# Kernel optimization log

Measured on AMD Instinct MI355X. Metric: run time of the kernel, lower is better.

Reference implementation:

```python
import jax, jax.numpy as jnp
import numpy as np

EPS = 1e-8
CLAMP = 1.0 - 1e-5
C = 1.0  # curvature


def _norm(x):
    return jnp.sqrt(jnp.sum(x * x, axis=-1, keepdims=True))


def clamp_to_ball(x, c=C):
    max_norm = CLAMP / c ** 0.5
    n = jnp.maximum(_norm(x), EPS)
    scale = jnp.where(n > max_norm, max_norm / n, 1.0)
    return x * scale


def logmap0(x, c=C):
    n = jnp.maximum(_norm(x), EPS)
    sc = c ** 0.5
    a = jnp.minimum(sc * n, 1.0 - EPS)
    return jnp.arctanh(a) / (sc * n) * x


def expmap0(v, c=C):
    n = jnp.maximum(_norm(v), EPS)
    sc = c ** 0.5
    t = jnp.minimum(sc * n, 15.0)
    return clamp_to_ball(jnp.tanh(t) * v / (sc * n), c)


def mobius_add(x, y, c=C):
    x2 = jnp.sum(x * x, -1, keepdims=True)
    y2 = jnp.sum(y * y, -1, keepdims=True)
    xy = jnp.sum(x * y, -1, keepdims=True)
    num = (1 + 2 * c * xy + c * y2) * x + (1 - c * x2) * y
    den = 1 + 2 * c * xy + c * c * x2 * y2
    return clamp_to_ball(num / jnp.maximum(den, EPS), c)


def hyp_linear(x, W, b, c=C):
    out = expmap0(logmap0(x, c) @ W.T, c)
    bias_ball = expmap0(b[None, :], c)
    return mobius_add(out, jnp.broadcast_to(bias_ball, out.shape), c)


def pairwise_poincare_dist(Q, K, c=C):
    # Q, K: [B, h, T, dk]. Distance d(q,k) = 2/sqrt(c) * atanh(sqrt(c)*||(-q) (+) k||).
    # ||num||^2 of mobius_add(-q, k) depends only on scalars |q|^2, |k|^2, q.k,
    # so we avoid the (B,h,T,T,dk) expansion while computing identical math.
    q2 = jnp.sum(Q * Q, -1)[..., :, None]          # [B,h,T,1]
    k2 = jnp.sum(K * K, -1)[..., None, :]          # [B,h,1,T]
    xy = -jnp.einsum('bhtd,bhsd->bhts', Q, K)      # (-q).k
    A = 1 + 2 * c * xy + c * k2
    Bc = 1 - c * q2
    num2 = A * A * q2 + Bc * Bc * k2 + 2 * A * Bc * xy
    den = jnp.maximum(1 + 2 * c * xy + c * c * q2 * k2, EPS)
    n = jnp.sqrt(jnp.maximum(num2, 0.0)) / den
    n = jnp.minimum(n, CLAMP / c ** 0.5)           # clamp_to_ball on the diff vector
    n = jnp.minimum(n, 1.0 - EPS)                  # .clamp(max=1-EPS)
    sc = c ** 0.5
    return 2.0 / sc * jnp.arctanh(sc * n)


def setup_inputs() -> dict:
    key = jax.random.key(0)
    ks = jax.random.split(key, 10)
    B, T, d = 4, 1024, 512
    x = expmap0(0.05 * jax.random.normal(ks[0], (B, T, d), jnp.float32))
    a = (6.0 / (d + d)) ** 0.5  # xavier uniform bound
    def w(k):
        return jax.random.uniform(k, (d, d), jnp.float32, -a, a)
    return {
        'x': x,
        'Wq': w(ks[1]), 'bq': 0.01 * jax.random.normal(ks[2], (d,), jnp.float32),
        'Wk': w(ks[3]), 'bk': 0.01 * jax.random.normal(ks[4], (d,), jnp.float32),
        'Wv': w(ks[5]), 'bv': 0.01 * jax.random.normal(ks[6], (d,), jnp.float32),
        'Wo': w(ks[7]), 'bo': 0.01 * jax.random.normal(ks[8], (d,), jnp.float32),
    }


def reference(x, Wq, bq, Wk, bk, Wv, bv, Wo, bo):
    B, T, d = x.shape
    h = 8
    dk = d // h
    x_eucl = logmap0(x, C)
    Q = hyp_linear(x, Wq, bq, C)
    K = hyp_linear(x, Wk, bk, C)
    V = x_eucl @ Wv.T + bv
    Q = Q.reshape(B, T, h, dk).transpose(0, 2, 1, 3)
    K = K.reshape(B, T, h, dk).transpose(0, 2, 1, 3)
    V = V.reshape(B, T, h, dk).transpose(0, 2, 1, 3)
    dists = pairwise_poincare_dist(Q, K, C)        # [B,h,T,T]
    scores = -dists / (dk ** 0.5)
    attn = jax.nn.softmax(scores, axis=-1)
    out = jnp.einsum('bhts,bhsd->bhtd', attn, V)
    out = out.transpose(0, 2, 1, 3).reshape(B, T, d)
    return out @ Wo.T + bo
```

## Files before the change

kernel.cpp:

```cpp
#include <hip/hip_runtime.h>
#include <math.h>

#define EPSF   1e-8f
#define CLAMPF 0.99999f

typedef __attribute__((ext_vector_type(8))) short bf16x8;
typedef __attribute__((ext_vector_type(4))) float f32x4;
#define MFMA16(a,b,c) __builtin_amdgcn_mfma_f32_16x16x32_bf16(a,b,c,0,0,0)

__device__ __forceinline__ unsigned cvt_pk_bf16(float lo, float hi) {
  unsigned r;
  asm("v_cvt_pk_bf16_f32 %0, %1, %2" : "=v"(r) : "v"(lo), "v"(hi));
  return r;
}

typedef __attribute__((address_space(1))) const void GV;
typedef __attribute__((address_space(3))) void LV;
__device__ __forceinline__ void gload_lds16(const void* g, void* l) {
  __builtin_amdgcn_global_load_lds((GV*)g, (LV*)l, 16, 0, 0);
}

__device__ __forceinline__ float wave_sum64(float v) {
  v += __shfl_xor(v, 1, 64);
  v += __shfl_xor(v, 2, 64);
  v += __shfl_xor(v, 4, 64);
  v += __shfl_xor(v, 8, 64);
  v += __shfl_xor(v, 16, 64);
  v += __shfl_xor(v, 32, 64);
  return v;
}

__global__ __launch_bounds__(256) void prep_logmap(const float* __restrict__ x,
                                                   const float* __restrict__ Wq,
                                                   const float* __restrict__ Wk,
                                                   const float* __restrict__ Wv,
                                                   const float* __restrict__ Wo,
                                                   const float* __restrict__ bq,
                                                   const float* __restrict__ bk,
                                                   short* __restrict__ xe,
                                                   short* __restrict__ Wqbf,
                                                   short* __restrict__ Wkbf,
                                                   short* __restrict__ Wvbf,
                                                   short* __restrict__ Wobf,
                                                   float* __restrict__ bb) {
  const int id = blockIdx.x;
  const int t = threadIdx.x;
  __shared__ float red[4];
  if (id < 2048) {
    const int half = t >> 7, tc = t & 127;
    const int row = id * 2 + half;
    float4 v = ((const float4*)(x + (size_t)row * 512))[tc];
    float s = wave_sum64(v.x * v.x + v.y * v.y + v.z * v.z + v.w * v.w);
    if ((t & 63) == 0) red[t >> 6] = s;
    __syncthreads();
    float n2 = red[half * 2] + red[half * 2 + 1];
    float n = sqrtf(n2);
    float nm = fmaxf(n, EPSF);
    float a = fminf(nm, 1.0f);
    float at = 0.5f * logf((1.f + a) / (1.f - a));
    float sc = at / nm;
    uint2 o;
    o.x = cvt_pk_bf16(v.x * sc, v.y * sc);
    o.y = cvt_pk_bf16(v.z * sc, v.w * sc);
    ((uint2*)(xe + (size_t)row * 512))[tc] = o;
    return;
  }
  const int wid = id - 2048;
  if (wid < 512) {
    const int which = wid >> 7, chunk = wid & 127;
    const float* src; short* dst;
    switch (which) {
      case 0: src = Wq; dst = Wqbf; break;
      case 1: src = Wk; dst = Wkbf; break;
      case 2: src = Wv; dst = Wvbf; break;
      default: src = Wo; dst = Wobf; break;
    }
    const int idx = chunk * 2048 + t * 8;
    float4 a = *(const float4*)(src + idx);
    float4 b2 = *(const float4*)(src + idx + 4);
    union { int4 v; unsigned u[4]; } o;
    o.u[0] = cvt_pk_bf16(a.x, a.y);
    o.u[1] = cvt_pk_bf16(a.z, a.w);
    o.u[2] = cvt_pk_bf16(b2.x, b2.y);
    o.u[3] = cvt_pk_bf16(b2.z, b2.w);
    *(int4*)(dst + idx) = o.v;
    return;
  }
  const int which = wid - 512;
  const float* b = which ? bk : bq;
  float* o = bb + (size_t)which * 520;
  float2 v = ((const float2*)b)[t];
  float s = wave_sum64(v.x * v.x + v.y * v.y);
  if ((t & 63) == 0) red[t >> 6] = s;
  __syncthreads();
  float n2 = red[0] + red[1] + red[2] + red[3];
  float n = sqrtf(n2);
  float nm = fmaxf(n, EPSF);
  float tt = fminf(nm, 15.f);
  float f = tanhf(tt) / nm;
  float on = f * nm;
  if (on > CLAMPF) f *= CLAMPF / on;
  ((float2*)o)[t] = make_float2(f * v.x, f * v.y);
  if (t == 0) o[512] = f * f * n2;
}

template <int VT>
__device__ __forceinline__ void gemm_core128(const short* __restrict__ A,
                                             const short* __restrict__ W,
                                             const float* __restrict__ bias,
                                             void* __restrict__ outp,
                                             int bx, int by) {
  __shared__ __align__(16) short As[128][64];
  __shared__ __align__(16) short Ws[64][64];
  const int t = threadIdx.x;
  const int wave = t >> 6, lane = t & 63, lg = lane >> 4, lr = lane & 15;
  const int mh = wave & 1, nh = wave >> 1;
  f32x4 z = {0.f, 0.f, 0.f, 0.f};
  f32x4 acc[4][2];
#pragma unroll
  for (int i = 0; i < 4; ++i) { acc[i][0] = z; acc[i][1] = z; }

  const int rsub = lane >> 3;
  const int swz = ((lane & 7) ^ rsub) * 8;
  const short* Ag0 = A + (size_t)(by * 128 + wave * 32 + rsub) * 512 + swz;
  const short* Wg0 = W + (size_t)(bx * 64 + wave * 16 + rsub) * 512 + swz;
  short* Al0 = &As[wave * 32][0];
  short* Al1 = &As[wave * 32 + 8][0];
  short* Al2 = &As[wave * 32 + 16][0];
  short* Al3 = &As[wave * 32 + 24][0];
  short* Wl0 = &Ws[wave * 16][0];
  short* Wl1 = &Ws[wave * 16 + 8][0];

  const int rb = nh * 32 + lr;
  const int cx = (lr & 7) * 8;

  for (int kt = 0; kt < 512; kt += 64) {
    __syncthreads();
    gload_lds16(Ag0 + kt, Al0);
    gload_lds16(Ag0 + kt + 8 * 512, Al1);
    gload_lds16(Ag0 + kt + 16 * 512, Al2);
    gload_lds16(Ag0 + kt + 24 * 512, Al3);
    gload_lds16(Wg0 + kt, Wl0);
    gload_lds16(Wg0 + kt + 8 * 512, Wl1);
    __syncthreads();
#pragma unroll
    for (int kk = 0; kk < 2; ++kk) {
      const int c = (kk * 32 + lg * 8) ^ cx;
      bf16x8 bf0 = *(const bf16x8*)&Ws[rb][c];
      bf16x8 bf1 = *(const bf16x8*)&Ws[rb + 16][c];
#pragma unroll
      for (int i = 0; i < 4; ++i) {
        bf16x8 af = *(const bf16x8*)&As[mh * 64 + i * 16 + lr][c];
        acc[i][0] = MFMA16(af, bf0, acc[i][0]);
        acc[i][1] = MFMA16(af, bf1, acc[i][1]);
      }
    }
  }

  if (VT == 0) {
    float* out = (float*)outp;
    float b0 = 0.f, b1 = 0.f;
    if (bias) { b0 = bias[bx * 64 + nh * 32 + lr]; b1 = bias[bx * 64 + nh * 32 + 16 + lr]; }
#pragma unroll
    for (int i = 0; i < 4; ++i) {
#pragma unroll
      for (int r = 0; r < 4; ++r) {
        size_t row = (size_t)(by * 128 + mh * 64 + i * 16 + lg * 4 + r);
        out[row * 512 + bx * 64 + nh * 32 + lr]      = acc[i][0][r] + b0;
        out[row * 512 + bx * 64 + nh * 32 + 16 + lr] = acc[i][1][r] + b1;
      }
    }
  } else {
    short* vt = (short*)outp;
    const int bidx = by >> 3;
    const int tokb = (by & 7) * 128 + mh * 64;
    const int c0 = bx * 64 + nh * 32 + lr;
    const int c1 = c0 + 16;
    const float b0 = bias[c0], b1 = bias[c1];
    size_t base0 = ((size_t)(bidx * 8 + (c0 >> 6)) * 64 + (c0 & 63)) * 1024;
    size_t base1 = ((size_t)(bidx * 8 + (c1 >> 6)) * 64 + (c1 & 63)) * 1024;
#pragma unroll
    for (int i = 0; i < 4; ++i) {
      const int tok0 = tokb + i * 16 + lg * 4;
      uint2 pk;
      pk.x = cvt_pk_bf16(acc[i][0][0] + b0, acc[i][0][1] + b0);
      pk.y = cvt_pk_bf16(acc[i][0][2] + b0, acc[i][0][3] + b0);
      *(uint2*)(vt + base0 + tok0) = pk;
      pk.x = cvt_pk_bf16(acc[i][1][0] + b1, acc[i][1][1] + b1);
      pk.y = cvt_pk_bf16(acc[i][1][2] + b1, acc[i][1][3] + b1);
      *(uint2*)(vt + base1 + tok0) = pk;
    }
  }
}

__device__ __forceinline__ void gemm_core64(const short* __restrict__ A,
                                            const short* __restrict__ W,
                                            const float* __restrict__ bias,
                                            float* __restrict__ out,
                                            int bx, int by) {
  __shared__ __align__(16) short As[64][64];
  __shared__ __align__(16) short Ws[64][64];
  const int t = threadIdx.x;
  const int wave = t >> 6, lane = t & 63, lg = lane >> 4, lr = lane & 15;
  const int mh = wave & 1, nh = wave >> 1;
  f32x4 z = {0.f, 0.f, 0.f, 0.f};
  f32x4 acc00 = z, acc01 = z, acc10 = z, acc11 = z;

  const int rsub = lane >> 3;
  const int swz = ((lane & 7) ^ rsub) * 8;
  const short* Ag0 = A + (size_t)(by * 64 + wave * 16 + rsub) * 512 + swz;
  const short* Ag1 = Ag0 + 8 * 512;
  const short* Wg0 = W + (size_t)(bx * 64 + wave * 16 + rsub) * 512 + swz;
  const short* Wg1 = Wg0 + 8 * 512;
  short* Al0 = &As[wave * 16][0];
  short* Al1 = &As[wave * 16 + 8][0];
  short* Wl0 = &Ws[wave * 16][0];
  short* Wl1 = &Ws[wave * 16 + 8][0];

  const int ra = mh * 32 + lr;
  const int rb = nh * 32 + lr;
  const int cx = (lr & 7) * 8;

  for (int kt = 0; kt < 512; kt += 64) {
    __syncthreads();
    gload_lds16(Ag0 + kt, Al0);
    gload_lds16(Ag1 + kt, Al1);
    gload_lds16(Wg0 + kt, Wl0);
    gload_lds16(Wg1 + kt, Wl1);
    __syncthreads();
#pragma unroll
    for (int kk = 0; kk < 2; ++kk) {
      const int c = (kk * 32 + lg * 8) ^ cx;
      bf16x8 af0 = *(const bf16x8*)&As[ra][c];
      bf16x8 af1 = *(const bf16x8*)&As[ra + 16][c];
      bf16x8 bf0 = *(const bf16x8*)&Ws[rb][c];
      bf16x8 bf1 = *(const bf16x8*)&Ws[rb + 16][c];
      acc00 = MFMA16(af0, bf0, acc00);
      acc01 = MFMA16(af0, bf1, acc01);
      acc10 = MFMA16(af1, bf0, acc10);
      acc11 = MFMA16(af1, bf1, acc11);
    }
  }

  float b0 = 0.f, b1 = 0.f;
  if (bias) { b0 = bias[bx * 64 + nh * 32 + lr]; b1 = bias[bx * 64 + nh * 32 + 16 + lr]; }
#pragma unroll
  for (int r = 0; r < 4; ++r) {
    size_t row0 = (size_t)(by * 64 + mh * 32 + lg * 4 + r);
    size_t row1 = row0 + 16;
    out[row0 * 512 + bx * 64 + nh * 32 + lr] = acc00[r] + b0;
    out[row0 * 512 + bx * 64 + nh * 32 + 16 + lr] = acc01[r] + b1;
    out[row1 * 512 + bx * 64 + nh * 32 + lr] = acc10[r] + b0;
    out[row1 * 512 + bx * 64 + nh * 32 + 16 + lr] = acc11[r] + b1;
  }
}

__global__ __launch_bounds__(256) void gemm_qkv(const short* __restrict__ A,
                                                const short* __restrict__ Wq,
                                                const short* __restrict__ Wk,
                                                const short* __restrict__ Wv,
                                                const float* __restrict__ bv,
                                                float* __restrict__ Qo,
                                                float* __restrict__ Ko,
                                                short* __restrict__ Vt) {
  switch (blockIdx.z) {
    case 0: gemm_core128<0>(A, Wq, nullptr, Qo, blockIdx.x, blockIdx.y); break;
    case 1: gemm_core128<0>(A, Wk, nullptr, Ko, blockIdx.x, blockIdx.y); break;
    default: gemm_core128<1>(A, Wv, bv, Vt, blockIdx.x, blockIdx.y); break;
  }
}

__global__ __launch_bounds__(256) void gemm_bf(const short* __restrict__ A,
                                               const short* __restrict__ W,
                                               const float* __restrict__ bias,
                                               float* __restrict__ out) {
  gemm_core64(A, W, bias, out, blockIdx.x, blockIdx.y);
}

__global__ __launch_bounds__(256) void hyp_epilogue_v4(const float* __restrict__ Qb,
                                                       const float* __restrict__ Kb,
                                                       const float* __restrict__ bbase,
                                                       short* __restrict__ Qbf,
                                                       short* __restrict__ Kbf,
                                                       float* __restrict__ q2h,
                                                       float* __restrict__ k2h) {
  const int which = blockIdx.y;
  const float* Y = which ? Kb : Qb;
  const float* bb = bbase + (size_t)which * 520;
  short* Ybf = which ? Kbf : Qbf;
  float* y2h = which ? k2h : q2h;
  const int t = threadIdx.x;
  const int half = t >> 7, tc = t & 127;
  const int row = blockIdx.x * 2 + half;

  float4 y = ((const float4*)(Y + (size_t)row * 512))[tc];
  float4 w = ((const float4*)bb)[tc];
  __shared__ float red[8];
  float sn = wave_sum64(y.x * y.x + y.y * y.y + y.z * y.z + y.w * y.w);
  float sd = wave_sum64(y.x * w.x + y.y * w.y + y.z * w.z + y.w * w.w);
  if ((t & 63) == 0) { red[t >> 6] = sn; red[4 + (t >> 6)] = sd; }
  __syncthreads();
  float n2 = red[half * 2] + red[half * 2 + 1];
  float dt = red[4 + half * 2] + red[4 + half * 2 + 1];
  float y2 = bb[512];
  float n = sqrtf(n2);
  float nm = fmaxf(n, EPSF);
  float tt = fminf(nm, 15.f);
  float f = tanhf(tt) / nm;
  float on = f * nm;
  if (on > CLAMPF) f *= CLAMPF / on;
  float x2 = f * f * n2;
  float xy = f * dt;
  float A = 1.f + 2.f * xy + y2;
  float Bc = 1.f - x2;
  float den = fmaxf(1.f + 2.f * xy + x2 * y2, EPSF);
  float num2 = A * A * x2 + Bc * Bc * y2 + 2.f * A * Bc * xy;
  float nn = sqrtf(fmaxf(num2, 0.f)) / den;
  float nnm = fmaxf(nn, EPSF);
  float s2 = (nnm > CLAMPF) ? (CLAMPF / nnm) : 1.f;
  float g = s2 / den;
  float ox = g * (A * f * y.x + Bc * w.x);
  float oy = g * (A * f * y.y + Bc * w.y);
  float oz = g * (A * f * y.z + Bc * w.z);
  float ow = g * (A * f * y.w + Bc * w.w);
  uint2 o;
  o.x = cvt_pk_bf16(ox, oy);
  o.y = cvt_pk_bf16(oz, ow);
  ((uint2*)(Ybf + (size_t)row * 512))[tc] = o;
  float hs = ox * ox + oy * oy + oz * oz + ow * ow;
  hs += __shfl_xor(hs, 1, 64);
  hs += __shfl_xor(hs, 2, 64);
  hs += __shfl_xor(hs, 4, 64);
  hs += __shfl_xor(hs, 8, 64);
  if ((tc & 15) == 0) y2h[(size_t)(tc >> 4) * 4096 + row] = hs;
}

__global__ __launch_bounds__(512, 2) void attn_mfma_v8(const short* __restrict__ Qbf,
                                                       const short* __restrict__ Kbf,
                                                       const float* __restrict__ q2h,
                                                       const float* __restrict__ k2h,
                                                       const short* __restrict__ Vt,
                                                       short* __restrict__ Obf) {
  __shared__ __align__(16) short Ks[64][72];
  __shared__ __align__(16) short Vs[64][72];
  __shared__ __align__(16) float k2s[64];
  __shared__ __align__(16) float Ls[4][16][68];
  __shared__ float lsb[4][16];

  const int t = threadIdx.x;
  const int id = blockIdx.x;
  const int qt = id >> 5;
  const int pr = (((id >> 3) & 3) << 3) | (id & 7);
  const int hd = pr & 7, b = pr >> 3;
  const int wave = t >> 6, lane = t & 63, lg = lane >> 4, lr = lane & 15;
  const int qh = wave >> 1, kh = wave & 1;

  const size_t qrow = (size_t)(b * 1024 + qt * 64 + qh * 16 + lr);
  const bf16x8 qf0 = *(const bf16x8*)(Qbf + qrow * 512 + hd * 64 + lg * 8);
  const bf16x8 qf1 = *(const bf16x8*)(Qbf + qrow * 512 + hd * 64 + 32 + lg * 8);

  const float q2 = q2h[(size_t)hd * 4096 + b * 1024 + qt * 64 + qh * 16 + lr];
  const float bc = 1.f - q2;
  const float q2p1 = 1.f + q2;
  const float Xmin = 0.125f * (-17.6096137f - __builtin_amdgcn_logf(bc));

  const int sr = t >> 3, q8 = t & 7;
  const int p32 = sr & 31;
  const int kwr = (sr & 32) | (((p32 >> 2) & 1) << 4) | (((p32 >> 3) & 3) << 2) | (p32 & 3);
  const short* kgp = Kbf + (size_t)(b * 1024 + sr) * 512 + hd * 64 + q8 * 8;
  const short* vgp = Vt + ((size_t)(b * 8 + hd) * 64 + sr) * 1024 + q8 * 8;
  const float* k2gp = k2h + (size_t)hd * 4096 + b * 1024 + t;

  int4 rk0 = *(const int4*)kgp;
  int4 rv0 = *(const int4*)vgp;
  float rk2 = (t < 64) ? (1.f - *k2gp) : 0.f;

  f32x4 z = {0.f, 0.f, 0.f, 0.f};
  f32x4 acc0 = z, acc1 = z, acc2 = z, acc3 = z;
  float ls = 0.f;
  const int krow = kh * 32 + lr;
  const int kcol = kh * 32 + lg * 8;

  for (int kt = 0; kt < 16; ++kt) {
    __syncthreads();
    *(int4*)&Ks[kwr][q8 * 8] = rk0;
    *(int4*)&Vs[sr][q8 * 8] = rv0;
    if (t < 64) k2s[t] = rk2;
    __syncthreads();
    if (kt < 15) {
      kgp += 64 * 512; vgp += 64; k2gp += 64;
      rk0 = *(const int4*)kgp;
      rv0 = *(const int4*)vgp;
      if (t < 64) rk2 = 1.f - *k2gp;
    }

    bf16x8 kf0 = *(const bf16x8*)&Ks[krow][lg * 8];
    bf16x8 kf1 = *(const bf16x8*)&Ks[krow][32 + lg * 8];
    bf16x8 kg0 = *(const bf16x8*)&Ks[krow + 16][lg * 8];
    bf16x8 kg1 = *(const bf16x8*)&Ks[krow + 16][32 + lg * 8];
    __builtin_amdgcn_s_setprio(1);
    f32x4 sA = MFMA16(kf0, qf0, z);
    sA = MFMA16(kf1, qf1, sA);
    f32x4 sB = MFMA16(kg0, qf0, z);
    sB = MFMA16(kg1, qf1, sB);
    __builtin_amdgcn_s_setprio(0);

    float pA[4], pB[4];
#pragma unroll
    for (int r = 0; r < 4; ++r) {
      float d = sA[r];
      float mk = k2s[kh * 32 + lg * 8 + r];
      float den = fmaxf(fmaf(-2.f, d, fmaf(-q2, mk, q2p1)), EPSF);
      float t1 = fmaxf(fmaf(-bc, mk, den), 0.f);
      float sq = __builtin_amdgcn_sqrtf(den * t1);
      float vv = den + sq;
      float wv = mk * den;
      float X = fmaf(0.125f, __builtin_amdgcn_logf(wv),
                     -0.25f * __builtin_amdgcn_logf(vv));
      pA[r] = __builtin_amdgcn_exp2f(fmaxf(X, Xmin));
    }
#pragma unroll
    for (int r = 0; r < 4; ++r) {
      float d = sB[r];
      float mk = k2s[kh * 32 + lg * 8 + 4 + r];
      float den = fmaxf(fmaf(-2.f, d, fmaf(-q2, mk, q2p1)), EPSF);
      float t1 = fmaxf(fmaf(-bc, mk, den), 0.f);
      float sq = __builtin_amdgcn_sqrtf(den * t1);
      float vv = den + sq;
      float wv = mk * den;
      float X = fmaf(0.125f, __builtin_amdgcn_logf(wv),
                     -0.25f * __builtin_amdgcn_logf(vv));
      pB[r] = __builtin_amdgcn_exp2f(fmaxf(X, Xmin));
    }
    ls += (pA[0] + pA[1] + pA[2] + pA[3]) + (pB[0] + pB[1] + pB[2] + pB[3]);

    union { unsigned u[4]; bf16x8 v; } pf;
    pf.u[0] = cvt_pk_bf16(pA[0], pA[1]);
    pf.u[1] = cvt_pk_bf16(pA[2], pA[3]);
    pf.u[2] = cvt_pk_bf16(pB[0], pB[1]);
    pf.u[3] = cvt_pk_bf16(pB[2], pB[3]);

    bf16x8 v0 = *(const bf16x8*)&Vs[lr][kcol];
    bf16x8 v1 = *(const bf16x8*)&Vs[16 + lr][kcol];
    bf16x8 v2 = *(const bf16x8*)&Vs[32 + lr][kcol];
    bf16x8 v3 = *(const bf16x8*)&Vs[48 + lr][kcol];
    __builtin_amdgcn_s_setprio(1);
    acc0 = MFMA16(v0, pf.v, acc0);
    acc1 = MFMA16(v1, pf.v, acc1);
    acc2 = MFMA16(v2, pf.v, acc2);
    acc3 = MFMA16(v3, pf.v, acc3);
    __builtin_amdgcn_s_setprio(0);
  }

  ls += __shfl_xor(ls, 16, 64);
  ls += __shfl_xor(ls, 32, 64);

  if (kh == 1) {
    float* Lq = &Ls[qh][lr][0];
    *(f32x4*)(Lq + lg * 4) = acc0;
    *(f32x4*)(Lq + 16 + lg * 4) = acc1;
    *(f32x4*)(Lq + 32 + lg * 4) = acc2;
    *(f32x4*)(Lq + 48 + lg * 4) = acc3;
    if (lg == 0) lsb[qh][lr] = ls;
  }
  __syncthreads();
  if (kh == 0) {
    const float* Lq = &Ls[qh][lr][0];
    acc0 += *(const f32x4*)(Lq + lg * 4);
    acc1 += *(const f32x4*)(Lq + 16 + lg * 4);
    acc2 += *(const f32x4*)(Lq + 32 + lg * 4);
    acc3 += *(const f32x4*)(Lq + 48 + lg * 4);
    float inv = 1.f / (ls + lsb[qh][lr]);
    short* ob = Obf + qrow * 512 + hd * 64 + lg * 4;
    uint2 pk;
    pk.x = cvt_pk_bf16(acc0[0] * inv, acc0[1] * inv);
    pk.y = cvt_pk_bf16(acc0[2] * inv, acc0[3] * inv);
    *(uint2*)(ob) = pk;
    pk.x = cvt_pk_bf16(acc1[0] * inv, acc1[1] * inv);
    pk.y = cvt_pk_bf16(acc1[2] * inv, acc1[3] * inv);
    *(uint2*)(ob + 16) = pk;
    pk.x = cvt_pk_bf16(acc2[0] * inv, acc2[1] * inv);
    pk.y = cvt_pk_bf16(acc2[2] * inv, acc2[3] * inv);
    *(uint2*)(ob + 32) = pk;
    pk.x = cvt_pk_bf16(acc3[0] * inv, acc3[1] * inv);
    pk.y = cvt_pk_bf16(acc3[2] * inv, acc3[3] * inv);
    *(uint2*)(ob + 48) = pk;
  }
}

extern "C" void kernel_launch(void* const* d_in, const int* in_sizes, int n_in,
                              void* d_out, int out_size, void* d_ws, size_t ws_size,
                              hipStream_t stream) {
  const float* x  = (const float*)d_in[0];
  const float* Wq = (const float*)d_in[1];
  const float* bq = (const float*)d_in[2];
  const float* Wk = (const float*)d_in[3];
  const float* bk = (const float*)d_in[4];
  const float* Wv = (const float*)d_in[5];
  const float* bv = (const float*)d_in[6];
  const float* Wo = (const float*)d_in[7];
  const float* bo = (const float*)d_in[8];
  float* out = (float*)d_out;
  float* ws  = (float*)d_ws;

  const size_t M1 = 1048576ull;
  float* Qb    = ws;
  float* Kb    = ws + 2 * M1;
  short* Vt    = (short*)(ws + 4 * M1);
  short* xe_bf = (short*)(ws + 5 * M1);
  short* Qbf   = (short*)(ws + 5 * M1);
  short* Wqbf  = (short*)(ws + 6 * M1);
  short* Wkbf  = (short*)(ws + 6 * M1 + 131072);
  short* Wvbf  = (short*)(ws + 6 * M1 + 262144);
  short* Wobf  = (short*)(ws + 6 * M1 + 393216);
  short* attn_out = (short*)(ws + 6 * M1 + 524288);
  short* Kbf = (short*)out;
  float* bb  = out + M1;
  float* q2h = out + M1 + 2048;
  float* k2h = out + M1 + 2048 + 32768;

  hipLaunchKernelGGL(prep_logmap, dim3(2562), dim3(256), 0, stream,
                     x, Wq, Wk, Wv, Wo, bq, bk, xe_bf, Wqbf, Wkbf, Wvbf, Wobf, bb);

  hipLaunchKernelGGL(gemm_qkv, dim3(8, 32, 3), dim3(256), 0, stream,
                     xe_bf, Wqbf, Wkbf, Wvbf, bv, Qb, Kb, Vt);

  hipLaunchKernelGGL(hyp_epilogue_v4, dim3(2048, 2), dim3(256), 0, stream,
                     Qb, Kb, bb, Qbf, Kbf, q2h, k2h);

  hipLaunchKernelGGL(attn_mfma_v8, dim3(512), dim3(512), 0, stream,
                     Qbf, Kbf, q2h, k2h, Vt, attn_out);

  hipLaunchKernelGGL(gemm_bf, dim3(8, 64), dim3(256), 0, stream, attn_out, Wobf, bo, out);
}
```

Before: 67.83 us.

## Give each attention wave two query sub-tiles to reuse K/V fragments

The attention kernel drops from 512 to 256 threads per block, and each wave now handles two 16-row query sub-tiles instead of one. Each K and V fragment read from shared memory therefore feeds twice as many MFMAs, and per-thread global loads double to cover the same 64x64 tile. This cuts LDS reads and waves per query tile but raises register pressure (eight accumulators) and leaves fewer waves per block to hide latency.

```diff
diff --git a/kernel.cpp b/kernel.cpp
--- a/kernel.cpp
+++ b/kernel.cpp
@@ -335,7 +335,7 @@
   if ((tc & 15) == 0) y2h[(size_t)(tc >> 4) * 4096 + row] = hs;
 }
 
-__global__ __launch_bounds__(512, 2) void attn_mfma_v8(const short* __restrict__ Qbf,
+__global__ __launch_bounds__(256, 4) void attn_mfma_v9(const short* __restrict__ Qbf,
                                                        const short* __restrict__ Kbf,
                                                        const float* __restrict__ q2h,
                                                        const float* __restrict__ k2h,
@@ -353,44 +353,55 @@
   const int pr = (((id >> 3) & 3) << 3) | (id & 7);
   const int hd = pr & 7, b = pr >> 3;
   const int wave = t >> 6, lane = t & 63, lg = lane >> 4, lr = lane & 15;
-  const int qh = wave >> 1, kh = wave & 1;
-
-  const size_t qrow = (size_t)(b * 1024 + qt * 64 + qh * 16 + lr);
-  const bf16x8 qf0 = *(const bf16x8*)(Qbf + qrow * 512 + hd * 64 + lg * 8);
-  const bf16x8 qf1 = *(const bf16x8*)(Qbf + qrow * 512 + hd * 64 + 32 + lg * 8);
-
-  const float q2 = q2h[(size_t)hd * 4096 + b * 1024 + qt * 64 + qh * 16 + lr];
-  const float bc = 1.f - q2;
-  const float q2p1 = 1.f + q2;
-  const float Xmin = 0.125f * (-17.6096137f - __builtin_amdgcn_logf(bc));
-
-  const int sr = t >> 3, q8 = t & 7;
+  const int qp = wave >> 1, kh = wave & 1;
+
+  const size_t qrow0 = (size_t)(b * 1024 + qt * 64 + qp * 32 + lr);
+  const bf16x8 qf00 = *(const bf16x8*)(Qbf + qrow0 * 512 + hd * 64 + lg * 8);
+  const bf16x8 qf01 = *(const bf16x8*)(Qbf + qrow0 * 512 + hd * 64 + 32 + lg * 8);
+  const bf16x8 qf10 = *(const bf16x8*)(Qbf + (qrow0 + 16) * 512 + hd * 64 + lg * 8);
+  const bf16x8 qf11 = *(const bf16x8*)(Qbf + (qrow0 + 16) * 512 + hd * 64 + 32 + lg * 8);
+
+  const float q2a = q2h[(size_t)hd * 4096 + b * 1024 + qt * 64 + qp * 32 + lr];
+  const float q2b = q2h[(size_t)hd * 4096 + b * 1024 + qt * 64 + qp * 32 + 16 + lr];
+  const float bcA = 1.f - q2a, bcB = 1.f - q2b;
+  const float q2p1A = 1.f + q2a, q2p1B = 1.f + q2b;
+  const float XminA = 0.125f * (-17.6096137f - __builtin_amdgcn_logf(bcA));
+  const float XminB = 0.125f * (-17.6096137f - __builtin_amdgcn_logf(bcB));
+
+  const int sr = t >> 2, q4 = t & 3;
   const int p32 = sr & 31;
   const int kwr = (sr & 32) | (((p32 >> 2) & 1) << 4) | (((p32 >> 3) & 3) << 2) | (p32 & 3);
-  const short* kgp = Kbf + (size_t)(b * 1024 + sr) * 512 + hd * 64 + q8 * 8;
-  const short* vgp = Vt + ((size_t)(b * 8 + hd) * 64 + sr) * 1024 + q8 * 8;
+  const short* kgp = Kbf + (size_t)(b * 1024 + sr) * 512 + hd * 64 + q4 * 16;
+  const short* vgp = Vt + ((size_t)(b * 8 + hd) * 64 + sr) * 1024 + q4 * 16;
   const float* k2gp = k2h + (size_t)hd * 4096 + b * 1024 + t;
 
   int4 rk0 = *(const int4*)kgp;
+  int4 rk1 = *(const int4*)(kgp + 8);
   int4 rv0 = *(const int4*)vgp;
+  int4 rv1 = *(const int4*)(vgp + 8);
   float rk2 = (t < 64) ? (1.f - *k2gp) : 0.f;
 
   f32x4 z = {0.f, 0.f, 0.f, 0.f};
-  f32x4 acc0 = z, acc1 = z, acc2 = z, acc3 = z;
-  float ls = 0.f;
+  f32x4 aA0 = z, aA1 = z, aA2 = z, aA3 = z;
+  f32x4 aB0 = z, aB1 = z, aB2 = z, aB3 = z;
+  float lsA = 0.f, lsB = 0.f;
   const int krow = kh * 32 + lr;
   const int kcol = kh * 32 + lg * 8;
 
   for (int kt = 0; kt < 16; ++kt) {
     __syncthreads();
-    *(int4*)&Ks[kwr][q8 * 8] = rk0;
-    *(int4*)&Vs[sr][q8 * 8] = rv0;
+    *(int4*)&Ks[kwr][q4 * 16] = rk0;
+    *(int4*)&Ks[kwr][q4 * 16 + 8] = rk1;
+    *(int4*)&Vs[sr][q4 * 16] = rv0;
+    *(int4*)&Vs[sr][q4 * 16 + 8] = rv1;
     if (t < 64) k2s[t] = rk2;
     __syncthreads();
     if (kt < 15) {
       kgp += 64 * 512; vgp += 64; k2gp += 64;
       rk0 = *(const int4*)kgp;
+      rk1 = *(const int4*)(kgp + 8);
       rv0 = *(const int4*)vgp;
+      rv1 = *(const int4*)(vgp + 8);
       if (t < 64) rk2 = 1.f - *k2gp;
     }
 
@@ -399,92 +410,147 @@
     bf16x8 kg0 = *(const bf16x8*)&Ks[krow + 16][lg * 8];
     bf16x8 kg1 = *(const bf16x8*)&Ks[krow + 16][32 + lg * 8];
     __builtin_amdgcn_s_setprio(1);
-    f32x4 sA = MFMA16(kf0, qf0, z);
-    sA = MFMA16(kf1, qf1, sA);
-    f32x4 sB = MFMA16(kg0, qf0, z);
-    sB = MFMA16(kg1, qf1, sB);
+    f32x4 sA0 = MFMA16(kf0, qf00, z);
+    sA0 = MFMA16(kf1, qf01, sA0);
+    f32x4 sB0 = MFMA16(kg0, qf00, z);
+    sB0 = MFMA16(kg1, qf01, sB0);
+    f32x4 sA1 = MFMA16(kf0, qf10, z);
+    sA1 = MFMA16(kf1, qf11, sA1);
+    f32x4 sB1 = MFMA16(kg0, qf10, z);
+    sB1 = MFMA16(kg1, qf11, sB1);
     __builtin_amdgcn_s_setprio(0);
 
-    float pA[4], pB[4];
+    float mkA[4], mkB[4];
 #pragma unroll
     for (int r = 0; r < 4; ++r) {
-      float d = sA[r];
-      float mk = k2s[kh * 32 + lg * 8 + r];
-      float den = fmaxf(fmaf(-2.f, d, fmaf(-q2, mk, q2p1)), EPSF);
-      float t1 = fmaxf(fmaf(-bc, mk, den), 0.f);
-      float sq = __builtin_amdgcn_sqrtf(den * t1);
-      float vv = den + sq;
-      float wv = mk * den;
-      float X = fmaf(0.125f, __builtin_amdgcn_logf(wv),
-                     -0.25f * __builtin_amdgcn_logf(vv));
-      pA[r] = __builtin_amdgcn_exp2f(fmaxf(X, Xmin));
-    }
+      mkA[r] = k2s[kh * 32 + lg * 8 + r];
+      mkB[r] = k2s[kh * 32 + lg * 8 + 4 + r];
+    }
+
+    float pA0[4], pB0[4], pA1[4], pB1[4];
 #pragma unroll
     for (int r = 0; r < 4; ++r) {
-      float d = sB[r];
-      float mk = k2s[kh * 32 + lg * 8 + 4 + r];
-      float den = fmaxf(fmaf(-2.f, d, fmaf(-q2, mk, q2p1)), EPSF);
-      float t1 = fmaxf(fmaf(-bc, mk, den), 0.f);
-      float sq = __builtin_amdgcn_sqrtf(den * t1);
-      float vv = den + sq;
-      float wv = mk * den;
-      float X = fmaf(0.125f, __builtin_amdgcn_logf(wv),
-                     -0.25f * __builtin_amdgcn_logf(vv));
-      pB[r] = __builtin_amdgcn_exp2f(fmaxf(X, Xmin));
-    }
-    ls += (pA[0] + pA[1] + pA[2] + pA[3]) + (pB[0] + pB[1] + pB[2] + pB[3]);
-
-    union { unsigned u[4]; bf16x8 v; } pf;
-    pf.u[0] = cvt_pk_bf16(pA[0], pA[1]);
-    pf.u[1] = cvt_pk_bf16(pA[2], pA[3]);
-    pf.u[2] = cvt_pk_bf16(pB[0], pB[1]);
-    pf.u[3] = cvt_pk_bf16(pB[2], pB[3]);
+      {
+        float den = fmaxf(fmaf(-2.f, sA0[r], fmaf(-q2a, mkA[r], q2p1A)), EPSF);
+        float t1 = fmaxf(fmaf(-bcA, mkA[r], den), 0.f);
+        float sq = __builtin_amdgcn_sqrtf(den * t1);
+        float X = fmaf(0.125f, __builtin_amdgcn_logf(mkA[r] * den),
+                       -0.25f * __builtin_amdgcn_logf(den + sq));
+        pA0[r] = __builtin_amdgcn_exp2f(fmaxf(X, XminA));
+      }
+      {
+        float den = fmaxf(fmaf(-2.f, sB0[r], fmaf(-q2a, mkB[r], q2p1A)), EPSF);
+        float t1 = fmaxf(fmaf(-bcA, mkB[r], den), 0.f);
+        float sq = __builtin_amdgcn_sqrtf(den * t1);
+        float X = fmaf(0.125f, __builtin_amdgcn_logf(mkB[r] * den),
+                       -0.25f * __builtin_amdgcn_logf(den + sq));
+        pB0[r] = __builtin_amdgcn_exp2f(fmaxf(X, XminA));
+      }
+      {
+        float den = fmaxf(fmaf(-2.f, sA1[r], fmaf(-q2b, mkA[r], q2p1B)), EPSF);
+        float t1 = fmaxf(fmaf(-bcB, mkA[r], den), 0.f);
+        float sq = __builtin_amdgcn_sqrtf(den * t1);
+        float X = fmaf(0.125f, __builtin_amdgcn_logf(mkA[r] * den),
+                       -0.25f * __builtin_amdgcn_logf(den + sq));
+        pA1[r] = __builtin_amdgcn_exp2f(fmaxf(X, XminB));
+      }
+      {
+        float den = fmaxf(fmaf(-2.f, sB1[r], fmaf(-q2b, mkB[r], q2p1B)), EPSF);
+        float t1 = fmaxf(fmaf(-bcB, mkB[r], den), 0.f);
+        float sq = __builtin_amdgcn_sqrtf(den * t1);
+        float X = fmaf(0.125f, __builtin_amdgcn_logf(mkB[r] * den),
+                       -0.25f * __builtin_amdgcn_logf(den + sq));
+        pB1[r] = __builtin_amdgcn_exp2f(fmaxf(X, XminB));
+      }
+    }
+    lsA += (pA0[0] + pA0[1] + pA0[2] + pA0[3]) + (pB0[0] + pB0[1] + pB0[2] + pB0[3]);
+    lsB += (pA1[0] + pA1[1] + pA1[2] + pA1[3]) + (pB1[0] + pB1[1] + pB1[2] + pB1[3]);
+
+    union { unsigned u[4]; bf16x8 v; } pf0, pf1;
+    pf0.u[0] = cvt_pk_bf16(pA0[0], pA0[1]);
+    pf0.u[1] = cvt_pk_bf16(pA0[2], pA0[3]);
+    pf0.u[2] = cvt_pk_bf16(pB0[0], pB0[1]);
+    pf0.u[3] = cvt_pk_bf16(pB0[2], pB0[3]);
+    pf1.u[0] = cvt_pk_bf16(pA1[0], pA1[1]);
+    pf1.u[1] = cvt_pk_bf16(pA1[2], pA1[3]);
+    pf1.u[2] = cvt_pk_bf16(pB1[0], pB1[1]);
+    pf1.u[3] = cvt_pk_bf16(pB1[2], pB1[3]);
 
     bf16x8 v0 = *(const bf16x8*)&Vs[lr][kcol];
     bf16x8 v1 = *(const bf16x8*)&Vs[16 + lr][kcol];
     bf16x8 v2 = *(const bf16x8*)&Vs[32 + lr][kcol];
     bf16x8 v3 = *(const bf16x8*)&Vs[48 + lr][kcol];
     __builtin_amdgcn_s_setprio(1);
-    acc0 = MFMA16(v0, pf.v, acc0);
-    acc1 = MFMA16(v1, pf.v, acc1);
-    acc2 = MFMA16(v2, pf.v, acc2);
-    acc3 = MFMA16(v3, pf.v, acc3);
+    aA0 = MFMA16(v0, pf0.v, aA0);
+    aA1 = MFMA16(v1, pf0.v, aA1);
+    aA2 = MFMA16(v2, pf0.v, aA2);
+    aA3 = MFMA16(v3, pf0.v, aA3);
+    aB0 = MFMA16(v0, pf1.v, aB0);
+    aB1 = MFMA16(v1, pf1.v, aB1);
+    aB2 = MFMA16(v2, pf1.v, aB2);
+    aB3 = MFMA16(v3, pf1.v, aB3);
     __builtin_amdgcn_s_setprio(0);
   }
 
-  ls += __shfl_xor(ls, 16, 64);
-  ls += __shfl_xor(ls, 32, 64);
+  lsA += __shfl_xor(lsA, 16, 64);
+  lsA += __shfl_xor(lsA, 32, 64);
+  lsB += __shfl_xor(lsB, 16, 64);
+  lsB += __shfl_xor(lsB, 32, 64);
 
   if (kh == 1) {
-    float* Lq = &Ls[qh][lr][0];
-    *(f32x4*)(Lq + lg * 4) = acc0;
-    *(f32x4*)(Lq + 16 + lg * 4) = acc1;
-    *(f32x4*)(Lq + 32 + lg * 4) = acc2;
-    *(f32x4*)(Lq + 48 + lg * 4) = acc3;
-    if (lg == 0) lsb[qh][lr] = ls;
+    float* Lq0 = &Ls[qp * 2][lr][0];
+    *(f32x4*)(Lq0 + lg * 4) = aA0;
+    *(f32x4*)(Lq0 + 16 + lg * 4) = aA1;
+    *(f32x4*)(Lq0 + 32 + lg * 4) = aA2;
+    *(f32x4*)(Lq0 + 48 + lg * 4) = aA3;
+    float* Lq1 = &Ls[qp * 2 + 1][lr][0];
+    *(f32x4*)(Lq1 + lg * 4) = aB0;
+    *(f32x4*)(Lq1 + 16 + lg * 4) = aB1;
+    *(f32x4*)(Lq1 + 32 + lg * 4) = aB2;
+    *(f32x4*)(Lq1 + 48 + lg * 4) = aB3;
+    if (lg == 0) { lsb[qp * 2][lr] = lsA; lsb[qp * 2 + 1][lr] = lsB; }
   }
   __syncthreads();
   if (kh == 0) {
-    const float* Lq = &Ls[qh][lr][0];
-    acc0 += *(const f32x4*)(Lq + lg * 4);
-    acc1 += *(const f32x4*)(Lq + 16 + lg * 4);
-    acc2 += *(const f32x4*)(Lq + 32 + lg * 4);
-    acc3 += *(const f32x4*)(Lq + 48 + lg * 4);
-    float inv = 1.f / (ls + lsb[qh][lr]);
-    short* ob = Obf + qrow * 512 + hd * 64 + lg * 4;
+    const float* Lq0 = &Ls[qp * 2][lr][0];
+    aA0 += *(const f32x4*)(Lq0 + lg * 4);
+    aA1 += *(const f32x4*)(Lq0 + 16 + lg * 4);
+    aA2 += *(const f32x4*)(Lq0 + 32 + lg * 4);
+    aA3 += *(const f32x4*)(Lq0 + 48 + lg * 4);
+    const float* Lq1 = &Ls[qp * 2 + 1][lr][0];
+    aB0 += *(const f32x4*)(Lq1 + lg * 4);
+    aB1 += *(const f32x4*)(Lq1 + 16 + lg * 4);
+    aB2 += *(const f32x4*)(Lq1 + 32 + lg * 4);
+    aB3 += *(const f32x4*)(Lq1 + 48 + lg * 4);
+    float invA = 1.f / (lsA + lsb[qp * 2][lr]);
+    float invB = 1.f / (lsB + lsb[qp * 2 + 1][lr]);
+    short* ob0 = Obf + qrow0 * 512 + hd * 64 + lg * 4;
+    short* ob1 = Obf + (qrow0 + 16) * 512 + hd * 64 + lg * 4;
     uint2 pk;
-    pk.x = cvt_pk_bf16(acc0[0] * inv, acc0[1] * inv);
-    pk.y = cvt_pk_bf16(acc0[2] * inv, acc0[3] * inv);
-    *(uint2*)(ob) = pk;
-    pk.x = cvt_pk_bf16(acc1[0] * inv, acc1[1] * inv);
-    pk.y = cvt_pk_bf16(acc1[2] * inv, acc1[3] * inv);
-    *(uint2*)(ob + 16) = pk;
-    pk.x = cvt_pk_bf16(acc2[0] * inv, acc2[1] * inv);
-    pk.y = cvt_pk_bf16(acc2[2] * inv, acc2[3] * inv);
-    *(uint2*)(ob + 32) = pk;
-    pk.x = cvt_pk_bf16(acc3[0] * inv, acc3[1] * inv);
-    pk.y = cvt_pk_bf16(acc3[2] * inv, acc3[3] * inv);
-    *(uint2*)(ob + 48) = pk;
+    pk.x = cvt_pk_bf16(aA0[0] * invA, aA0[1] * invA);
+    pk.y = cvt_pk_bf16(aA0[2] * invA, aA0[3] * invA);
+    *(uint2*)(ob0) = pk;
+    pk.x = cvt_pk_bf16(aA1[0] * invA, aA1[1] * invA);
+    pk.y = cvt_pk_bf16(aA1[2] * invA, aA1[3] * invA);
+    *(uint2*)(ob0 + 16) = pk;
+    pk.x = cvt_pk_bf16(aA2[0] * invA, aA2[1] * invA);
+    pk.y = cvt_pk_bf16(aA2[2] * invA, aA2[3] * invA);
+    *(uint2*)(ob0 + 32) = pk;
+    pk.x = cvt_pk_bf16(aA3[0] * invA, aA3[1] * invA);
+    pk.y = cvt_pk_bf16(aA3[2] * invA, aA3[3] * invA);
+    *(uint2*)(ob0 + 48) = pk;
+    pk.x = cvt_pk_bf16(aB0[0] * invB, aB0[1] * invB);
+    pk.y = cvt_pk_bf16(aB0[2] * invB, aB0[3] * invB);
+    *(uint2*)(ob1) = pk;
+    pk.x = cvt_pk_bf16(aB1[0] * invB, aB1[1] * invB);
+    pk.y = cvt_pk_bf16(aB1[2] * invB, aB1[3] * invB);
+    *(uint2*)(ob1 + 16) = pk;
+    pk.x = cvt_pk_bf16(aB2[0] * invB, aB2[1] * invB);
+    pk.y = cvt_pk_bf16(aB2[2] * invB, aB2[3] * invB);
+    *(uint2*)(ob1 + 32) = pk;
+    pk.x = cvt_pk_bf16(aB3[0] * invB, aB3[1] * invB);
+    pk.y = cvt_pk_bf16(aB3[2] * invB, aB3[3] * invB);
+    *(uint2*)(ob1 + 48) = pk;
   }
 }
 
@@ -528,7 +594,7 @@
   hipLaunchKernelGGL(hyp_epilogue_v4, dim3(2048, 2), dim3(256), 0, stream,
                      Qb, Kb, bb, Qbf, Kbf, q2h, k2h);
 
-  hipLaunchKernelGGL(attn_mfma_v8, dim3(512), dim3(512), 0, stream,
+  hipLaunchKernelGGL(attn_mfma_v9, dim3(512), dim3(256), 0, stream,
                      Qbf, Kbf, q2h, k2h, Vt, attn_out);
 
   hipLaunchKernelGGL(gemm_bf, dim3(8, 64), dim3(256), 0, stream, attn_out, Wobf, bo, out);
```

Result: slower. 70.76 us (+4.3%).
